# Performance work log

Measured on AMD Instinct MI355X. Metric: run time of the kernel, lower is better.

## Reference

```python
import jax, jax.numpy as jnp
import numpy as np

B, S, DIN, DOUT = 4, 2048, 4096, 4096

def setup_inputs() -> dict:
    key = jax.random.key(0)
    k1, k2, k3, k4 = jax.random.split(key, 4)
    x = jax.random.normal(k1, (B, S, DIN), dtype=jnp.float32)
    # int8 per-channel quantized weight (stored here as int32 holding int8 range values)
    weight = jax.random.randint(k2, (DOUT, DIN), -127, 128, dtype=jnp.int32)
    weight_scale = jax.random.uniform(k3, (DOUT,), dtype=jnp.float32, minval=0.001, maxval=0.02)
    weight_offset = jax.random.randint(k4, (DOUT,), -8, 8, dtype=jnp.int32)
    return {"x": x, "weight": weight, "weight_scale": weight_scale, "weight_offset": weight_offset}

def reference(x, weight, weight_scale, weight_offset):
    # W8A16 weight-only dequant: per-output-channel (w - offset) * scale, then GEMM.
    w_fp = (weight.astype(x.dtype) - weight_offset.astype(x.dtype)[:, None]) * weight_scale.astype(x.dtype)[:, None]  # [DOUT, DIN]
    # [B,S,DIN] @ [DOUT,DIN]^T -> [B,S,DOUT]
    return jnp.einsum('bsd,od->bso', x, w_fp)
```

## Files before the change

### kernel.cpp

```cpp
#include <hip/hip_runtime.h>
#include <stdint.h>

#define DIN   4096
#define DOUT  4096
#define MTOT  8192
#define NT    64

#define BM    256
#define BN    256
#define GRID_M (MTOT / BM)
#define GRID_N (DOUT / BN)
#define NWG   (GRID_M * GRID_N)

typedef __attribute__((ext_vector_type(4)))  float        f32x4;
typedef __attribute__((ext_vector_type(16))) float        f32x16;
typedef __attribute__((ext_vector_type(4)))  int          i32x4;
typedef __attribute__((ext_vector_type(4)))  unsigned int u32x4;
typedef __attribute__((ext_vector_type(2)))  unsigned int u32x2;
typedef __attribute__((ext_vector_type(8)))  short        bf16x8;

__device__ __forceinline__ unsigned int pack_bf2_rne(float a, float b) {
  unsigned int ua = __builtin_bit_cast(unsigned int, a);
  unsigned int ub = __builtin_bit_cast(unsigned int, b);
  ua += 0x7fffu + ((ua >> 16) & 1u);
  ub += 0x7fffu + ((ub >> 16) & 1u);
  return (ua >> 16) | (ub & 0xffff0000u);
}

__device__ __forceinline__ unsigned int pack_bf2_exact(int a, int b) {
  unsigned int ua = __builtin_bit_cast(unsigned int, (float)a);
  unsigned int ub = __builtin_bit_cast(unsigned int, (float)b);
  return (ua >> 16) | (ub & 0xffff0000u);
}

#define UNITS_A (GRID_M * 2 * NT)
#define UNITS_B (GRID_N * 2 * NT)
__global__ __launch_bounds__(256) void conv_kernel(const float* __restrict__ X,
                                                   u32x4* __restrict__ wsA,
                                                   const int* __restrict__ W,
                                                   const int* __restrict__ Off,
                                                   u32x4* __restrict__ wsB) {
  const int totA = UNITS_A * 1024;
  const int totB = UNITS_B * 1024;
  for (int idx = blockIdx.x * 256 + threadIdx.x; idx < totA + totB;
       idx += gridDim.x * 256) {
    if (idx < totA) {
      const int pos = idx & 1023;
      const int row = pos >> 3, ch = pos & 7;
      const int unit = idx >> 10;
      const int kt = unit & (NT - 1), rb = unit >> 6;
      const int m = rb * 128 + row;
      const f32x4* src = (const f32x4*)(X + ((long)m << 12) + kt * 64 + ch * 8);
      f32x4 f0 = src[0], f1 = src[1];
      u32x4 d;
      d[0] = pack_bf2_rne(f0[0], f0[1]);
      d[1] = pack_bf2_rne(f0[2], f0[3]);
      d[2] = pack_bf2_rne(f1[0], f1[1]);
      d[3] = pack_bf2_rne(f1[2], f1[3]);
      wsA[(long)unit * 1024 + ch * 128 + row] = d;
    } else {
      const int j = idx - totA;
      const int pos = j & 1023;
      const int row = pos >> 3, ch = pos & 7;
      const int unit = j >> 10;
      const int kt = unit & (NT - 1), nb = unit >> 6;
      const int n = nb * 128 + row;
      const i32x4* src = (const i32x4*)(W + ((long)n << 12) + kt * 64 + ch * 8);
      const int off = Off[n];
      i32x4 w0 = src[0], w1 = src[1];
      u32x4 d;
      d[0] = pack_bf2_exact(w0[0] - off, w0[1] - off);
      d[1] = pack_bf2_exact(w0[2] - off, w0[3] - off);
      d[2] = pack_bf2_exact(w1[0] - off, w1[1] - off);
      d[3] = pack_bf2_exact(w1[2] - off, w1[3] - off);
      wsB[(long)unit * 1024 + ch * 128 + row] = d;
    }
  }
}


#define BAR()   __builtin_amdgcn_s_barrier()
#define SB()    __builtin_amdgcn_sched_barrier(0)
#define LGKM_(N) asm volatile("s_waitcnt lgkmcnt(" #N ")" ::: "memory")
#define LGKM(N)  LGKM_(N)
#define WAITV(N) asm volatile("s_waitcnt vmcnt(" #N ")" ::: "memory")

typedef __attribute__((address_space(3))) const char* ldsp;

#define DSR(dst, p, IMM) \
  asm volatile("ds_read_b128 %0, %1 offset:" #IMM : "=v"(dst) : "v"(p))

#define STAGE(ldsArr, bufc, h, basePtr, t)                                      \
  { const u32x4* s_ = (basePtr) + (long)(t) * 1024;                             \
    _Pragma("unroll")                                                           \
    for (int i_ = 0; i_ < 2; ++i_) {                                            \
      const int o_ = tid + i_ * 512;                                            \
      __builtin_amdgcn_global_load_lds(                                         \
          (const __attribute__((address_space(1))) void*)(s_ + o_),             \
          (__attribute__((address_space(3))) void*)(&ldsArr[bufc][h][0] + o_),  \
          16, 0, 0);                                                            \
    } }

#define RD_B8(pB_)                                                              \
  DSR(bR[0][0], pB_, 0);     DSR(bR[0][1], pB_, 512);                           \
  DSR(bR[1][0], pB_, 4096);  DSR(bR[1][1], pB_, 4608);                          \
  DSR(bR[2][0], pB_, 8192);  DSR(bR[2][1], pB_, 8704);                          \
  DSR(bR[3][0], pB_, 12288); DSR(bR[3][1], pB_, 12800);
#define RD_A4(pA_, O0, O1, O2, O3)                                              \
  DSR(aR[0], pA_, O0); DSR(aR[1], pA_, O1);                                     \
  DSR(aR[2], pA_, O2); DSR(aR[3], pA_, O3);

#define MMA2(kk, mt)                                                            \
  acc[mt][0] = __builtin_amdgcn_mfma_f32_32x32x16_bf16(aR[kk], bR[kk][0],       \
                                                       acc[mt][0], 0, 0, 0);    \
  acc[mt][1] = __builtin_amdgcn_mfma_f32_32x32x16_bf16(aR[kk], bR[kk][1],       \
                                                       acc[mt][1], 0, 0, 0);

#define CASC(mt)                                                                \
  __builtin_amdgcn_s_setprio(1);                                                \
  LGKM(3); SB(); MMA2(0, mt)                                                    \
  LGKM(2); SB(); MMA2(1, mt)                                                    \
  LGKM(1); SB(); MMA2(2, mt)                                                    \
  LGKM(0); SB(); MMA2(3, mt)                                                    \
  __builtin_amdgcn_s_setprio(0);

#define TILE(pA_, pB_, ABUF, BBUF, t, SA, SBf, WV)                              \
  RD_B8(pB_) RD_A4(pA_, 0, 4096, 8192, 12288)                                   \
  if (SA) { STAGE(ldsA, ABUF, 0, bA0, (t) + 1) }                                \
  CASC(0) BAR();                                                                \
  RD_A4(pA_, 512, 4608, 8704, 12800)                                            \
  if (SA) { STAGE(ldsA, ABUF, 1, bA1, (t) + 1) }                                \
  CASC(1) BAR();                                                                \
  RD_A4(pA_, 1024, 5120, 9216, 13312)                                           \
  if (SBf) { STAGE(ldsB, BBUF, 0, bB0, (t) + 2) }                               \
  CASC(2) BAR();                                                                \
  RD_A4(pA_, 1536, 5632, 9728, 13824)                                           \
  if (SBf) { STAGE(ldsB, BBUF, 1, bB1, (t) + 2) }                               \
  WV; CASC(3) BAR();

__global__ __launch_bounds__(512, 2) void gemm8_kernel(
    const u32x4* __restrict__ wsA, const u32x4* __restrict__ wsB,
    const float* __restrict__ Scale, float* __restrict__ Out) {
  __shared__ u32x4 ldsA[2][2][1024];
  __shared__ u32x4 ldsB[2][2][1024];

  const int tid  = threadIdx.x;
  const int lane = tid & 63;
  const int wid  = tid >> 6;
  const int wr   = wid >> 2;
  const int wc   = wid & 3;
  const int wch  = wc >> 1;
  const int lane31 = lane & 31;
  const int lhi    = lane >> 5;

  int gid = (int)blockIdx.x;
  gid = (gid & 7) * (NWG >> 3) + (gid >> 3);
  const int wg_m = gid / GRID_N;
  const int wg_n = gid % GRID_N;

  const int lanepA = lane31 * 16 + lhi * 2048;
  const int lanepB = (wc & 1) * 1024 + lane31 * 16 + lhi * 2048;

  ldsp pA0 = (ldsp)((const char*)&ldsA[0][wr][0] + lanepA);
  ldsp pA1 = (ldsp)((const char*)&ldsA[1][wr][0] + lanepA);
  ldsp pB0 = (ldsp)((const char*)&ldsB[0][wch][0] + lanepB);
  ldsp pB1 = (ldsp)((const char*)&ldsB[1][wch][0] + lanepB);

  const u32x4* bA0 = wsA + (long)(wg_m * 2 + 0) * NT * 1024;
  const u32x4* bA1 = wsA + (long)(wg_m * 2 + 1) * NT * 1024;
  const u32x4* bB0 = wsB + (long)(wg_n * 2 + 0) * NT * 1024;
  const u32x4* bB1 = wsB + (long)(wg_n * 2 + 1) * NT * 1024;

  f32x16 acc[4][2];
#pragma unroll
  for (int m = 0; m < 4; ++m)
#pragma unroll
    for (int n = 0; n < 2; ++n)
#pragma unroll
      for (int q = 0; q < 16; ++q) acc[m][n][q] = 0.f;

  bf16x8 aR[4], bR[4][2];

  STAGE(ldsB, 0, 0, bB0, 0) STAGE(ldsA, 0, 0, bA0, 0)
  STAGE(ldsB, 0, 1, bB1, 0) STAGE(ldsA, 0, 1, bA1, 0)
  STAGE(ldsB, 1, 0, bB0, 1) STAGE(ldsB, 1, 1, bB1, 1)
  WAITV(4); BAR();

#pragma unroll 1
  for (int it = 0; it < 31; ++it) {
    const int t = 2 * it;
    TILE(pA0, pB0, 1, 0, t,     1, 1, WAITV(4))
    TILE(pA1, pB1, 0, 1, t + 1, 1, 1, WAITV(4))
  }
  TILE(pA0, pB0, 1, 0, 62, 1, 0, WAITV(0))
  TILE(pA1, pB1, 0, 1, 63, 0, 0, )

  const int col0 = wg_n * BN + wc * 64 + lane31;
  const int row0 = wg_m * BM + wr * 128 + lhi * 4;
#pragma unroll
  for (int nt = 0; nt < 2; ++nt) {
    const int col = col0 + nt * 32;
    const float s = Scale[col];
#pragma unroll
    for (int mt = 0; mt < 4; ++mt) {
      const int rb = row0 + mt * 32;
#pragma unroll
      for (int q = 0; q < 4; ++q)
#pragma unroll
        for (int j = 0; j < 4; ++j)
          Out[(long)(rb + q * 8 + j) * DOUT + col] = acc[mt][nt][q * 4 + j] * s;
    }
  }
}

__global__ __launch_bounds__(256, 2) void gemm_fused_kernel(
    const float* __restrict__ X, const int* __restrict__ W,
    const int* __restrict__ Off, const float* __restrict__ Scale,
    float* __restrict__ Out) {
  __shared__ char ldsA[2][128 * 64 * 2];
  __shared__ char ldsB[2][128 * 64 * 2];

  const int tid  = threadIdx.x;
  const int lane = tid & 63;
  const int wid  = tid >> 6;
  const int fwr  = wid >> 1;
  const int fwc  = wid & 1;

  int gid = (int)blockIdx.x;
  gid = (gid & 7) * (2048 >> 3) + (gid >> 3);
  const int wg_m = gid / 32;
  const int wg_n = gid % 32;
  const int brow = wg_m * 128;
  const int bcol = wg_n * 128;

  f32x4 acc[4][4];
#pragma unroll
  for (int m = 0; m < 4; ++m)
#pragma unroll
    for (int n = 0; n < 4; ++n) acc[m][n] = (f32x4){0.f, 0.f, 0.f, 0.f};

  int aoff[2][4], boff[2][4];
#pragma unroll
  for (int kk = 0; kk < 2; ++kk)
#pragma unroll
    for (int m = 0; m < 4; ++m) {
      const int kb = kk * 64 + ((lane >> 4) << 4);
      const int ra = fwr * 64 + m * 16 + (lane & 15);
      const int rb = fwc * 64 + m * 16 + (lane & 15);
      aoff[kk][m] = ra * 128 + (kb ^ ((ra & 7) << 4));
      boff[kk][m] = rb * 128 + (kb ^ ((rb & 7) << 4));
    }

  long xo[8], wo[8];
  int lo[8], ofv[8];
#pragma unroll
  for (int i = 0; i < 8; ++i) {
    const int idx = tid + i * 256;
    const int row = idx >> 4, c4 = idx & 15;
    xo[i] = (long)(brow + row) * DIN + c4 * 4;
    wo[i] = (long)(bcol + row) * DIN + c4 * 4;
    lo[i] = row * 128 + ((c4 * 8) ^ ((row & 7) << 4));
    ofv[i] = Off[bcol + row];
  }
  {
#pragma unroll
    for (int i = 0; i < 8; ++i) {
      f32x4 f = *(const f32x4*)(X + xo[i]);
      u32x2 d;
      d[0] = pack_bf2_rne(f[0], f[1]);
      d[1] = pack_bf2_rne(f[2], f[3]);
      *(u32x2*)(&ldsA[0][lo[i]]) = d;
    }
#pragma unroll
    for (int i = 0; i < 8; ++i) {
      i32x4 w = *(const i32x4*)(W + wo[i]);
      u32x2 d;
      d[0] = pack_bf2_exact(w[0] - ofv[i], w[1] - ofv[i]);
      d[1] = pack_bf2_exact(w[2] - ofv[i], w[3] - ofv[i]);
      *(u32x2*)(&ldsB[0][lo[i]]) = d;
    }
  }
  __syncthreads();
#pragma unroll 1
  for (int kt = 0; kt < NT; ++kt) {
    const int cur = kt & 1;
    const bool pf = (kt + 1 < NT);
    f32x4 fa[8];
    i32x4 fb[8];
    if (pf) {
      const int ko = (kt + 1) * 64;
#pragma unroll
      for (int i = 0; i < 8; ++i) fa[i] = *(const f32x4*)(X + xo[i] + ko);
#pragma unroll
      for (int i = 0; i < 8; ++i) fb[i] = *(const i32x4*)(W + wo[i] + ko);
    }
#pragma unroll
    for (int kk = 0; kk < 2; ++kk) {
      bf16x8 fa2[4], fb2[4];
#pragma unroll
      for (int m = 0; m < 4; ++m)
        fa2[m] = __builtin_bit_cast(bf16x8, *(const u32x4*)(&ldsA[cur][aoff[kk][m]]));
#pragma unroll
      for (int n = 0; n < 4; ++n)
        fb2[n] = __builtin_bit_cast(bf16x8, *(const u32x4*)(&ldsB[cur][boff[kk][n]]));
#pragma unroll
      for (int m = 0; m < 4; ++m)
#pragma unroll
        for (int n = 0; n < 4; ++n)
          acc[m][n] = __builtin_amdgcn_mfma_f32_16x16x32_bf16(fa2[m], fb2[n], acc[m][n], 0, 0, 0);
    }
    if (pf) {
      char* dA = ldsA[cur ^ 1];
      char* dB = ldsB[cur ^ 1];
#pragma unroll
      for (int i = 0; i < 8; ++i) {
        u32x2 d;
        d[0] = pack_bf2_rne(fa[i][0], fa[i][1]);
        d[1] = pack_bf2_rne(fa[i][2], fa[i][3]);
        *(u32x2*)(&dA[lo[i]]) = d;
      }
#pragma unroll
      for (int i = 0; i < 8; ++i) {
        u32x2 d;
        d[0] = pack_bf2_exact(fb[i][0] - ofv[i], fb[i][1] - ofv[i]);
        d[1] = pack_bf2_exact(fb[i][2] - ofv[i], fb[i][3] - ofv[i]);
        *(u32x2*)(&dB[lo[i]]) = d;
      }
    }
    __syncthreads();
  }

  const int col0 = bcol + fwc * 64 + (lane & 15);
  const int row0 = brow + fwr * 64 + ((lane >> 4) << 2);
#pragma unroll
  for (int n = 0; n < 4; ++n) {
    const int col = col0 + n * 16;
    const float s = Scale[col];
#pragma unroll
    for (int m = 0; m < 4; ++m) {
      const int r = row0 + m * 16;
#pragma unroll
      for (int j = 0; j < 4; ++j)
        Out[(long)(r + j) * DOUT + col] = acc[m][n][j] * s;
    }
  }
}

extern "C" void kernel_launch(void* const* d_in, const int* in_sizes, int n_in,
                              void* d_out, int out_size, void* d_ws, size_t ws_size,
                              hipStream_t stream) {
  (void)in_sizes; (void)n_in; (void)out_size;
  const float* X  = (const float*)d_in[0];
  const int*   W  = (const int*)d_in[1];
  const float* Sc = (const float*)d_in[2];
  const int*   Of = (const int*)d_in[3];
  float* Out = (float*)d_out;

  const size_t needA = (size_t)MTOT * DIN * 2;
  const size_t needB = (size_t)DOUT * DIN * 2;
  if (ws_size >= needA + needB) {
    u32x4* wsA = (u32x4*)d_ws;
    u32x4* wsB = (u32x4*)((char*)d_ws + needA);
    conv_kernel<<<3072, 256, 0, stream>>>(X, wsA, W, Of, wsB);
    gemm8_kernel<<<NWG, 512, 0, stream>>>(wsA, wsB, Sc, Out);
  } else {
    gemm_fused_kernel<<<2048, 256, 0, stream>>>(X, W, Of, Sc, Out);
  }
}
```

Before: 277.9 us.

## Load B operand directly from global into registers, bypassing LDS

The B (weight) tile no longer goes through LDS staging. Each wave loads its B fragments straight into registers with global_load_dwordx4, one tile ahead, and the k-loop is reordered so the outer cascade iterates over k-slices. The aim is to cut LDS traffic and LDS footprint, and to drop the B ds_reads. The cost is extra global/L2 traffic, because waves sharing a column half each fetch the same B data, plus more vmcnt waits and register pressure from the in-flight B registers.

```diff
diff --git a/kernel.cpp b/kernel.cpp
--- a/kernel.cpp
+++ b/kernel.cpp
@@ -90,59 +90,66 @@
 #define DSR(dst, p, IMM) \
   asm volatile("ds_read_b128 %0, %1 offset:" #IMM : "=v"(dst) : "v"(p))
 
-#define STAGE(ldsArr, bufc, h, basePtr, t)                                      \
+#define STAGE(bufc, h, basePtr, t)                                              \
   { const u32x4* s_ = (basePtr) + (long)(t) * 1024;                             \
     _Pragma("unroll")                                                           \
     for (int i_ = 0; i_ < 2; ++i_) {                                            \
       const int o_ = tid + i_ * 512;                                            \
       __builtin_amdgcn_global_load_lds(                                         \
           (const __attribute__((address_space(1))) void*)(s_ + o_),             \
-          (__attribute__((address_space(3))) void*)(&ldsArr[bufc][h][0] + o_),  \
+          (__attribute__((address_space(3))) void*)(&ldsA[bufc][h][0] + o_),    \
           16, 0, 0);                                                            \
     } }
 
-#define RD_B8(pB_)                                                              \
-  DSR(bR[0][0], pB_, 0);     DSR(bR[0][1], pB_, 512);                           \
-  DSR(bR[1][0], pB_, 4096);  DSR(bR[1][1], pB_, 4608);                          \
-  DSR(bR[2][0], pB_, 8192);  DSR(bR[2][1], pB_, 8704);                          \
-  DSR(bR[3][0], pB_, 12288); DSR(bR[3][1], pB_, 12800);
+#define BLOAD(kk, t)                                                            \
+  { const char* pk_ = bBw + (long)((t) + 1) * 16384 + (kk) * 4096;              \
+    asm volatile("global_load_dwordx4 %0, %1, off"                              \
+                 : "=v"(bR[kk][0]) : "v"(pk_));                                 \
+    asm volatile("global_load_dwordx4 %0, %1, off offset:512"                   \
+                 : "=v"(bR[kk][1]) : "v"(pk_)); }
+
 #define RD_A4(pA_, O0, O1, O2, O3)                                              \
   DSR(aR[0], pA_, O0); DSR(aR[1], pA_, O1);                                     \
   DSR(aR[2], pA_, O2); DSR(aR[3], pA_, O3);
 
-#define MMA2(kk, mt)                                                            \
-  acc[mt][0] = __builtin_amdgcn_mfma_f32_32x32x16_bf16(aR[kk], bR[kk][0],       \
+#define MMA2(mt, kk)                                                            \
+  acc[mt][0] = __builtin_amdgcn_mfma_f32_32x32x16_bf16(aR[mt], bR[kk][0],       \
                                                        acc[mt][0], 0, 0, 0);    \
-  acc[mt][1] = __builtin_amdgcn_mfma_f32_32x32x16_bf16(aR[kk], bR[kk][1],       \
+  acc[mt][1] = __builtin_amdgcn_mfma_f32_32x32x16_bf16(aR[mt], bR[kk][1],       \
                                                        acc[mt][1], 0, 0, 0);
 
-#define CASC(mt)                                                                \
+#define CASC(kk)                                                                \
   __builtin_amdgcn_s_setprio(1);                                                \
-  LGKM(3); SB(); MMA2(0, mt)                                                    \
-  LGKM(2); SB(); MMA2(1, mt)                                                    \
-  LGKM(1); SB(); MMA2(2, mt)                                                    \
-  LGKM(0); SB(); MMA2(3, mt)                                                    \
+  LGKM(3); SB(); MMA2(0, kk)                                                    \
+  LGKM(2); SB(); MMA2(1, kk)                                                    \
+  LGKM(1); SB(); MMA2(2, kk)                                                    \
+  LGKM(0); SB(); MMA2(3, kk)                                                    \
   __builtin_amdgcn_s_setprio(0);
 
-#define TILE(pA_, pB_, ABUF, BBUF, t, SA, SBf, WV)                              \
-  RD_B8(pB_) RD_A4(pA_, 0, 4096, 8192, 12288)                                   \
-  if (SA) { STAGE(ldsA, ABUF, 0, bA0, (t) + 1) }                                \
-  CASC(0) BAR();                                                                \
-  RD_A4(pA_, 512, 4608, 8704, 12800)                                            \
-  if (SA) { STAGE(ldsA, ABUF, 1, bA1, (t) + 1) }                                \
-  CASC(1) BAR();                                                                \
-  RD_A4(pA_, 1024, 5120, 9216, 13312)                                           \
-  if (SBf) { STAGE(ldsB, BBUF, 0, bB0, (t) + 2) }                               \
-  CASC(2) BAR();                                                                \
-  RD_A4(pA_, 1536, 5632, 9728, 13824)                                           \
-  if (SBf) { STAGE(ldsB, BBUF, 1, bB1, (t) + 2) }                               \
-  WV; CASC(3) BAR();
+#define TILE(pA_, ABUF, t, SG, W1, W2, W3, WE)                                  \
+  RD_A4(pA_, 0, 512, 1024, 1536)                                                \
+  if (SG) { STAGE(ABUF, 0, bA0, (t) + 1) }                                      \
+  CASC(0)                                                                       \
+  if (SG) { BLOAD(0, t) }                                                       \
+  BAR();                                                                        \
+  RD_A4(pA_, 4096, 4608, 5120, 5632)                                            \
+  if (SG) { STAGE(ABUF, 1, bA1, (t) + 1) }                                      \
+  W1; CASC(1)                                                                   \
+  if (SG) { BLOAD(1, t) }                                                       \
+  BAR();                                                                        \
+  RD_A4(pA_, 8192, 8704, 9216, 9728)                                            \
+  W2; CASC(2)                                                                   \
+  if (SG) { BLOAD(2, t) }                                                       \
+  BAR();                                                                        \
+  RD_A4(pA_, 12288, 12800, 13312, 13824)                                        \
+  W3; CASC(3)                                                                   \
+  if (SG) { BLOAD(3, t) }                                                       \
+  WE; BAR();
 
 __global__ __launch_bounds__(512, 2) void gemm8_kernel(
     const u32x4* __restrict__ wsA, const u32x4* __restrict__ wsB,
     const float* __restrict__ Scale, float* __restrict__ Out) {
   __shared__ u32x4 ldsA[2][2][1024];
-  __shared__ u32x4 ldsB[2][2][1024];
 
   const int tid  = threadIdx.x;
   const int lane = tid & 63;
@@ -150,6 +157,7 @@
   const int wr   = wid >> 2;
   const int wc   = wid & 3;
   const int wch  = wc >> 1;
+  const int wcl  = wc & 1;
   const int lane31 = lane & 31;
   const int lhi    = lane >> 5;
 
@@ -159,17 +167,14 @@
   const int wg_n = gid % GRID_N;
 
   const int lanepA = lane31 * 16 + lhi * 2048;
-  const int lanepB = (wc & 1) * 1024 + lane31 * 16 + lhi * 2048;
 
   ldsp pA0 = (ldsp)((const char*)&ldsA[0][wr][0] + lanepA);
   ldsp pA1 = (ldsp)((const char*)&ldsA[1][wr][0] + lanepA);
-  ldsp pB0 = (ldsp)((const char*)&ldsB[0][wch][0] + lanepB);
-  ldsp pB1 = (ldsp)((const char*)&ldsB[1][wch][0] + lanepB);
 
   const u32x4* bA0 = wsA + (long)(wg_m * 2 + 0) * NT * 1024;
   const u32x4* bA1 = wsA + (long)(wg_m * 2 + 1) * NT * 1024;
-  const u32x4* bB0 = wsB + (long)(wg_n * 2 + 0) * NT * 1024;
-  const u32x4* bB1 = wsB + (long)(wg_n * 2 + 1) * NT * 1024;
+  const char* bBw = (const char*)(wsB + (long)(wg_n * 2 + wch) * NT * 1024)
+                  + wcl * 1024 + lane31 * 16 + lhi * 2048;
 
   f32x16 acc[4][2];
 #pragma unroll
@@ -181,19 +186,18 @@
 
   bf16x8 aR[4], bR[4][2];
 
-  STAGE(ldsB, 0, 0, bB0, 0) STAGE(ldsA, 0, 0, bA0, 0)
-  STAGE(ldsB, 0, 1, bB1, 0) STAGE(ldsA, 0, 1, bA1, 0)
-  STAGE(ldsB, 1, 0, bB0, 1) STAGE(ldsB, 1, 1, bB1, 1)
-  WAITV(4); BAR();
+  STAGE(0, 0, bA0, 0) STAGE(0, 1, bA1, 0)
+  BLOAD(0, -1) BLOAD(1, -1) BLOAD(2, -1) BLOAD(3, -1)
+  WAITV(6); BAR();
 
 #pragma unroll 1
   for (int it = 0; it < 31; ++it) {
     const int t = 2 * it;
-    TILE(pA0, pB0, 1, 0, t,     1, 1, WAITV(4))
-    TILE(pA1, pB1, 0, 1, t + 1, 1, 1, WAITV(4))
-  }
-  TILE(pA0, pB0, 1, 0, 62, 1, 0, WAITV(0))
-  TILE(pA1, pB1, 0, 1, 63, 0, 0, )
+    TILE(pA0, 1, t,     1, WAITV(10), WAITV(10), WAITV(10), WAITV(6))
+    TILE(pA1, 0, t + 1, 1, WAITV(10), WAITV(10), WAITV(10), WAITV(6))
+  }
+  TILE(pA0, 1, 62, 1, WAITV(10), WAITV(10), WAITV(10), WAITV(6))
+  TILE(pA1, 0, 63, 0, WAITV(4),  WAITV(2),  WAITV(0),  )
 
   const int col0 = wg_n * BN + wc * 64 + lane31;
   const int row0 = wg_m * BM + wr * 128 + lhi * 4;
```

Result: slower. 284.1 us (+2.2%).
